# Optimization experiments

Hardware: AMD Instinct MI355X
Metric: run time of the kernel (lower is better)

The kernel has to match this reference:

```python
import jax, jax.numpy as jnp
import numpy as np

N_HEADS = 16
D_EMBED = 1024
N_CROSS = 768
D_HEAD = D_EMBED // N_HEADS


def setup_inputs() -> dict:
    key = jax.random.key(0)
    ks = jax.random.split(key, 10)
    B, S = 2, 2048
    x = jax.random.normal(ks[0], (B, S, D_EMBED), dtype=jnp.float32)
    context = jax.random.normal(ks[1], (B, S, N_CROSS), dtype=jnp.float32)
    sq = 1.0 / np.sqrt(D_EMBED)
    sc = 1.0 / np.sqrt(N_CROSS)
    Wq = jax.random.normal(ks[2], (D_EMBED, D_EMBED), dtype=jnp.float32) * sq
    bq = jnp.zeros((D_EMBED,), dtype=jnp.float32)
    Wk = jax.random.normal(ks[3], (N_CROSS, D_EMBED), dtype=jnp.float32) * sc
    bk = jnp.zeros((D_EMBED,), dtype=jnp.float32)
    Wv = jax.random.normal(ks[4], (N_CROSS, D_EMBED), dtype=jnp.float32) * sc
    bv = jnp.zeros((D_EMBED,), dtype=jnp.float32)
    Wo = jax.random.normal(ks[5], (D_EMBED, D_EMBED), dtype=jnp.float32) * sq
    bo = jnp.zeros((D_EMBED,), dtype=jnp.float32)
    return {"x": x, "context": context, "Wq": Wq, "bq": bq, "Wk": Wk, "bk": bk,
            "Wv": Wv, "bv": bv, "Wo": Wo, "bo": bo}


def reference(x, context, Wq, bq, Wk, bk, Wv, bv, Wo, bo):
    B, S, _ = x.shape

    def split_heads(t):  # [B,S,E] -> [B,H,S,Dh]
        return t.reshape(B, S, N_HEADS, D_HEAD).transpose(0, 2, 1, 3)

    q = split_heads(x @ Wq + bq)
    k = split_heads(context @ Wk + bk)
    v = split_heads(context @ Wv + bv)

    scale = 1.0 / np.sqrt(D_HEAD)
    scores = jnp.einsum('bhqd,bhkd->bhqk', q, k) * scale
    attn = jax.nn.softmax(scores, axis=-1)
    out = jnp.einsum('bhqk,bhkd->bhqd', attn, v)
    out = out.transpose(0, 2, 1, 3).reshape(B, S, D_EMBED)
    return out @ Wo + bo
```

## Files before the change

### kernel.cpp

```cpp
#include <hip/hip_runtime.h>
#include <math.h>


namespace {

typedef short bfr __attribute__((ext_vector_type(8)));
typedef short s4v __attribute__((ext_vector_type(4)));
typedef unsigned u4v __attribute__((ext_vector_type(4)));
typedef float accf __attribute__((ext_vector_type(16)));

#define MFMA32(a, b, c) __builtin_amdgcn_mfma_f32_32x32x16_bf16(a, b, c, 0, 0, 0)

__device__ inline short f2bf(float f) {
    unsigned u = __float_as_uint(f);
    u += 0x7fffu + ((u >> 16) & 1u);
    return (short)(u >> 16);
}
__device__ inline float bf2f(short s) {
    return __uint_as_float(((unsigned)(unsigned short)s) << 16);
}
__device__ inline float fexp2(float x) { return __builtin_amdgcn_exp2f(x); }
__device__ inline accf zero16() {
    accf z;
#pragma unroll
    for (int i = 0; i < 16; ++i) z[i] = 0.f;
    return z;
}
__device__ inline void dma16(const void* g, void* l) {
    __builtin_amdgcn_global_load_lds(
        (const __attribute__((address_space(1))) void*)g,
        (__attribute__((address_space(3))) void*)l, 16, 0, 0);
}

__global__ __launch_bounds__(256) void prep(
    const float* __restrict__ x, const float* __restrict__ ctx,
    short* __restrict__ xb, short* __restrict__ cb,
    const float* __restrict__ Wq, const float* __restrict__ Wk,
    const float* __restrict__ Wv, const float* __restrict__ Wo,
    short* __restrict__ Wqt, short* __restrict__ Wkt,
    short* __restrict__ Wvt, short* __restrict__ Wot) {
    __shared__ short t[64][68];
    const int bx = blockIdx.x;
    if (bx < 7168) {
        int i = bx * 256 + threadIdx.x;
        if (i < 1048576) {
            float4 v = ((const float4*)x)[i];
            s4v p = {f2bf(v.x), f2bf(v.y), f2bf(v.z), f2bf(v.w)};
            ((s4v*)xb)[i] = p;
        } else {
            int j = i - 1048576;
            float4 v = ((const float4*)ctx)[j];
            s4v p = {f2bf(v.x), f2bf(v.y), f2bf(v.z), f2bf(v.w)};
            ((s4v*)cb)[j] = p;
        }
        return;
    }
    const int idx = bx - 7168;
    const int z = idx >> 8, gy = (idx >> 4) & 15, gx = idx & 15;
    const float* W;
    short* Wt;
    int K;
    switch (z) {
        case 0: W = Wq; Wt = Wqt; K = 1024; break;
        case 1: W = Wk; Wt = Wkt; K = 768; break;
        case 2: W = Wv; Wt = Wvt; K = 768; break;
        default: W = Wo; Wt = Wot; K = 1024; break;
    }
    const int k0 = gy * 64;
    if (k0 >= K) return;
    const int tid = threadIdx.x;
    const int n0 = gx * 64;
    const int kr = tid >> 4, nc = (tid & 15) * 4;
#pragma unroll
    for (int rep = 0; rep < 4; ++rep) {
        int k = kr + rep * 16;
        float4 v = *(const float4*)&W[(size_t)(k0 + k) * 1024 + n0 + nc];
        t[nc + 0][k] = f2bf(v.x);
        t[nc + 1][k] = f2bf(v.y);
        t[nc + 2][k] = f2bf(v.z);
        t[nc + 3][k] = f2bf(v.w);
    }
    __syncthreads();
    const int nr = tid >> 4, kc = (tid & 15) * 4;
#pragma unroll
    for (int rep = 0; rep < 4; ++rep) {
        int n = nr + rep * 16;
        s4v p = {t[n][kc], t[n][kc + 1], t[n][kc + 2], t[n][kc + 3]};
        *(s4v*)&Wt[(size_t)(n0 + n) * K + k0 + kc] = p;
    }
}

__global__ __launch_bounds__(512, 6) void gemm_qkv(
    const short* __restrict__ xb, const short* __restrict__ cb,
    const short* __restrict__ Wqt, const short* __restrict__ Wkt,
    const short* __restrict__ Wvt, const float* __restrict__ bq,
    const float* __restrict__ bk, const float* __restrict__ bv,
    short* __restrict__ Qf, short* __restrict__ Kf, short* __restrict__ Vt,
    float qscale) {
    const int bid = blockIdx.x;
    const int z = bid >> 8;
    const int local = bid & 255;
    const short* A  = (z == 0) ? xb : cb;
    const short* Bt = (z == 0) ? Wqt : ((z == 1) ? Wkt : Wvt);
    const float* bias = (z == 0) ? bq : ((z == 1) ? bk : bv);
    const int K = (z == 0) ? 1024 : 768;
    const int NIT = K / 32;
    const float scale = (z == 0) ? qscale : 1.f;
    short* out = (z == 0) ? Qf : ((z == 1) ? Kf : Vt);

    __shared__ short As[12288];
    __shared__ short Bs[12288];
    const int t = threadIdx.x, lane = t & 63, w = t >> 6;
    const int lm = lane & 31, h2 = lane >> 5;
    const int wm = w & 1, wn = w >> 1;
    const int m0 = (local & 31) * 128, n0 = (local >> 5) * 128;

    const int st = t ^ ((t >> 3) & 7);
    const int srow = st >> 2, scol = (st & 3) * 8;
    const short* ga = A + (size_t)(m0 + srow) * K + scol;
    const short* gb = Bt + (size_t)(n0 + srow) * K + scol;

    const int xorv = (lm >> 1) & 7;
    const int rA0 = wm * 64 + lm, rB0 = wn * 32 + lm;

    accf acc[2] = {zero16(), zero16()};

    dma16(ga, &As[w * 512]);
    dma16(gb, &Bs[w * 512]);
    __builtin_amdgcn_sched_barrier(0);
    dma16(ga + 32, &As[4096 + w * 512]);
    dma16(gb + 32, &Bs[4096 + w * 512]);
    __builtin_amdgcn_sched_barrier(0);

    int buf = 0;
#pragma unroll 1
    for (int it = 0; it < NIT; ++it) {
        __builtin_amdgcn_sched_barrier(0);
        asm volatile("s_waitcnt vmcnt(2)" ::: "memory");
        __builtin_amdgcn_s_barrier();
        __builtin_amdgcn_sched_barrier(0);
        {
            const int nx = (it + 2 >= NIT) ? (it + 2 - NIT) : (it + 2);
            const int nb = (buf + 2 >= 3) ? (buf - 1) : (buf + 2);
            dma16(ga + nx * 32, &As[nb * 4096 + w * 512]);
            dma16(gb + nx * 32, &Bs[nb * 4096 + w * 512]);
        }
        const short* bA = &As[buf * 4096];
        const short* bB = &Bs[buf * 4096];
#pragma unroll
        for (int kk8 = 0; kk8 < 4; kk8 += 2) {
            bfr a0 = *(const bfr*)&bA[((rA0 * 4 + h2 + kk8) ^ xorv) * 8];
            bfr a1 = *(const bfr*)&bA[(((rA0 + 32) * 4 + h2 + kk8) ^ xorv) * 8];
            bfr b0 = *(const bfr*)&bB[((rB0 * 4 + h2 + kk8) ^ xorv) * 8];
            acc[0] = MFMA32(a0, b0, acc[0]);
            acc[1] = MFMA32(a1, b0, acc[1]);
        }
        buf = (buf + 1 == 3) ? 0 : buf + 1;
    }
    asm volatile("s_waitcnt vmcnt(0)" ::: "memory");
    __builtin_amdgcn_sched_barrier(0);

    const int n = n0 + wn * 32 + lm;
    const float bn = bias[n];
    const int hh = n >> 6, dd = n & 63;
#pragma unroll
    for (int mt = 0; mt < 2; ++mt) {
        const int mbase = m0 + wm * 64 + mt * 32 + 4 * h2;
        if (z != 2) {
            const int cb2 = (dd >> 4) * 512 + ((dd >> 3) & 1) * 256 + (dd & 7);
#pragma unroll
            for (int r = 0; r < 16; ++r) {
                const int m = mbase + (r & 3) + 8 * (r >> 2);
                const int bb = m >> 11, q = m & 2047;
                float v = (acc[mt][r] + bn) * scale;
                out[((size_t)((bb * 16 + hh) * 64 + (q >> 5))) * 2048 +
                    cb2 + (q & 31) * 8] = f2bf(v);
            }
        } else {
            const int dblk = dd >> 5, lmv = dd & 31;
#pragma unroll
            for (int g = 0; g < 4; ++g) {
                const int m = mbase + 8 * g;
                const int bb = m >> 11, s = m & 2047;
                const int kvt = s >> 6, kc = (s >> 4) & 3;
                const int h2v = (s >> 3) & 1, j0 = s & 7;
                s4v pq = {f2bf(acc[mt][4 * g + 0] + bn),
                          f2bf(acc[mt][4 * g + 1] + bn),
                          f2bf(acc[mt][4 * g + 2] + bn),
                          f2bf(acc[mt][4 * g + 3] + bn)};
                *(s4v*)(out +
                        ((size_t)(((bb * 16 + hh) * 32 + kvt) * 2 + dblk)) * 2048 +
                        kc * 512 + h2v * 256 + lmv * 8 + j0) = pq;
            }
        }
    }
}

__global__ __launch_bounds__(256) void combine(
    short* __restrict__ p0, const short* __restrict__ p1,
    const float* __restrict__ lsum) {
    const int i = blockIdx.x * 256 + threadIdx.x;
    const size_t gi = (size_t)i * 8;
    const int row = (int)(gi >> 10), col = (int)(gi & 1023);
    const int h = col >> 6;
    const int b = row >> 11, q = row & 2047;
    const float l0 = lsum[((size_t)b * 16 + h) * 2048 + q];
    const float l1 = lsum[((size_t)(2 + b) * 16 + h) * 2048 + q];
    const float iv = 1.f / (l0 + l1);
    bfr v0 = *(const bfr*)(p0 + gi);
    bfr v1 = *(const bfr*)(p1 + gi);
    bfr pk;
#pragma unroll
    for (int j = 0; j < 8; ++j)
        pk[j] = f2bf((bf2f(v0[j]) + bf2f(v1[j])) * iv);
    *(bfr*)(p0 + gi) = pk;
}

__global__ __launch_bounds__(512, 6) void gemm_o(
    const short* __restrict__ Af, const short* __restrict__ Bt,
    const float* __restrict__ bias, float* __restrict__ out) {
    constexpr int K = 1024, NIT = 32;
    __shared__ short As[12288];
    __shared__ short Bs[12288];
    const int t = threadIdx.x, lane = t & 63, w = t >> 6;
    const int lm = lane & 31, h2 = lane >> 5;
    const int wm = w & 1, wn = w >> 1;
    const int bid = blockIdx.x;
    const int m0 = (bid & 31) * 128, n0 = (bid >> 5) * 128;

    const int st = t ^ ((t >> 3) & 7);
    const int srow = st >> 2, scol = (st & 3) * 8;
    const short* ga = Af + (size_t)(m0 + srow) * K + scol;
    const short* gb = Bt + (size_t)(n0 + srow) * K + scol;

    const int xorv = (lm >> 1) & 7;
    const int rA0 = wm * 64 + lm, rB0 = wn * 32 + lm;

    accf acc[2] = {zero16(), zero16()};

    dma16(ga, &As[w * 512]);
    dma16(gb, &Bs[w * 512]);
    __builtin_amdgcn_sched_barrier(0);
    dma16(ga + 32, &As[4096 + w * 512]);
    dma16(gb + 32, &Bs[4096 + w * 512]);
    __builtin_amdgcn_sched_barrier(0);

    int buf = 0;
#pragma unroll 1
    for (int it = 0; it < NIT; ++it) {
        __builtin_amdgcn_sched_barrier(0);
        asm volatile("s_waitcnt vmcnt(2)" ::: "memory");
        __builtin_amdgcn_s_barrier();
        __builtin_amdgcn_sched_barrier(0);
        {
            const int nx = (it + 2 >= NIT) ? (it + 2 - NIT) : (it + 2);
            const int nb = (buf + 2 >= 3) ? (buf - 1) : (buf + 2);
            dma16(ga + nx * 32, &As[nb * 4096 + w * 512]);
            dma16(gb + nx * 32, &Bs[nb * 4096 + w * 512]);
        }
        const short* bA = &As[buf * 4096];
        const short* bB = &Bs[buf * 4096];
#pragma unroll
        for (int kk8 = 0; kk8 < 4; kk8 += 2) {
            bfr a0 = *(const bfr*)&bA[((rA0 * 4 + h2 + kk8) ^ xorv) * 8];
            bfr a1 = *(const bfr*)&bA[(((rA0 + 32) * 4 + h2 + kk8) ^ xorv) * 8];
            bfr b0 = *(const bfr*)&bB[((rB0 * 4 + h2 + kk8) ^ xorv) * 8];
            acc[0] = MFMA32(a0, b0, acc[0]);
            acc[1] = MFMA32(a1, b0, acc[1]);
        }
        buf = (buf + 1 == 3) ? 0 : buf + 1;
    }
    asm volatile("s_waitcnt vmcnt(0)" ::: "memory");
    __builtin_amdgcn_sched_barrier(0);

    const int n = n0 + wn * 32 + lm;
    const float bn = bias[n];
#pragma unroll
    for (int mt = 0; mt < 2; ++mt) {
        const int mbase = m0 + wm * 64 + mt * 32 + 4 * h2;
#pragma unroll
        for (int r = 0; r < 16; ++r) {
            const int m = mbase + (r & 3) + 8 * (r >> 2);
            out[(size_t)m * 1024 + n] = acc[mt][r] + bn;
        }
    }
}

__global__ __launch_bounds__(256, 3) void attn(
    const short* __restrict__ Qf, const short* __restrict__ Kf,
    const short* __restrict__ Vt, short* __restrict__ part,
    float* __restrict__ lsum) {
    __shared__ short smem[16384];
    const int bid = blockIdx.x;
    const int hidx = bid & 31, qs = bid >> 5;
    const int split = qs & 1, qb = qs >> 1;
    const int b = hidx >> 4, h = hidx & 15;
    const int lane = threadIdx.x & 63, wv = threadIdx.x >> 6;
    const int lm = lane & 31, h2 = lane >> 5;
    const bool hb = h2 != 0;
    const int q0 = qb * 128 + wv * 32;

    const short* qbase =
        Qf + ((size_t)(hidx * 64 + (q0 >> 5))) * 2048 + lane * 8;
    bfr qf[4];
#pragma unroll
    for (int kc = 0; kc < 4; ++kc) qf[kc] = *(const bfr*)(qbase + kc * 512);

    const short* khead = Kf + (size_t)hidx * 131072 + split * 65536;
    const short* vhead = Vt + (size_t)hidx * 131072 + split * 65536;
    const short* gsrc =
        ((wv < 2) ? (khead + wv * 2048) : (vhead + (wv - 2) * 2048)) + lane * 8;

#pragma unroll
    for (int i = 0; i < 4; ++i)
        dma16(gsrc + i * 512, &smem[wv * 2048 + i * 512]);

    accf oa0 = zero16(), oa1 = zero16();
    float la0 = 0.f, la1 = 0.f;

#pragma unroll 1
    for (int it = 0; it < 16; ++it) {
        const int p = it & 1;
        __syncthreads();
        if (it + 1 < 16) {
            const short* gn = gsrc + (size_t)(it + 1) * 4096;
            short* ln = &smem[(1 - p) * 8192 + wv * 2048];
#pragma unroll
            for (int i = 0; i < 4; ++i) dma16(gn + i * 512, ln + i * 512);
        }
        const short* kb = &smem[p * 8192];
        bfr kf0[4], kf1[4], vf0[4], vf1[4];
#pragma unroll
        for (int kc = 0; kc < 4; ++kc) {
            kf0[kc] = *(const bfr*)&kb[kc * 512 + lane * 8];
            kf1[kc] = *(const bfr*)&kb[2048 + kc * 512 + lane * 8];
            vf0[kc] = *(const bfr*)&kb[4096 + kc * 512 + lane * 8];
            vf1[kc] = *(const bfr*)&kb[6144 + kc * 512 + lane * 8];
        }
        accf s0 = zero16(), s1 = zero16();
#pragma unroll
        for (int kc = 0; kc < 4; ++kc) {
            s0 = MFMA32(kf0[kc], qf[kc], s0);
            s1 = MFMA32(kf1[kc], qf[kc], s1);
        }

#pragma unroll
        for (int i = 0; i < 16; ++i) s0[i] = fexp2(s0[i]);
#pragma unroll
        for (int i = 0; i < 16; ++i) s1[i] = fexp2(s1[i]);
#pragma unroll
        for (int i = 0; i < 16; ++i) {
            if (i & 1) la1 += s0[i] + s1[i];
            else       la0 += s0[i] + s1[i];
        }

        bfr pb[4];
#pragma unroll
        for (int kc = 0; kc < 4; ++kc) {
            const accf& s = (kc < 2) ? s0 : s1;
            const int base = 8 * (kc & 1);
            unsigned Lw0 = __builtin_amdgcn_perm(__float_as_uint(s[base + 1]),
                                                 __float_as_uint(s[base + 0]),
                                                 0x07060302u);
            unsigned Lw1 = __builtin_amdgcn_perm(__float_as_uint(s[base + 3]),
                                                 __float_as_uint(s[base + 2]),
                                                 0x07060302u);
            unsigned Hw0 = __builtin_amdgcn_perm(__float_as_uint(s[base + 5]),
                                                 __float_as_uint(s[base + 4]),
                                                 0x07060302u);
            unsigned Hw1 = __builtin_amdgcn_perm(__float_as_uint(s[base + 7]),
                                                 __float_as_uint(s[base + 6]),
                                                 0x07060302u);
            unsigned c0 = hb ? Lw0 : Hw0;
            unsigned c1 = hb ? Lw1 : Hw1;
            unsigned r0 = (unsigned)__shfl_xor((int)c0, 32);
            unsigned r1 = (unsigned)__shfl_xor((int)c1, 32);
            u4v pw = {hb ? r0 : Lw0, hb ? r1 : Lw1,
                      hb ? Hw0 : r0, hb ? Hw1 : r1};
            pb[kc] = __builtin_bit_cast(bfr, pw);
        }

#pragma unroll
        for (int kc = 0; kc < 4; ++kc) {
            oa0 = MFMA32(vf0[kc], pb[kc], oa0);
            oa1 = MFMA32(vf1[kc], pb[kc], oa1);
        }
    }

    float ls = la0 + la1;
    ls += __shfl_xor(ls, 32);
    if (!hb) lsum[((size_t)(split * 2 + b) * 16 + h) * 2048 + q0 + lm] = ls;

    short* orow = part + (size_t)split * 4194304 +
                  (size_t)(b * 2048 + q0 + lm) * 1024 + h * 64;
#pragma unroll
    for (int dt = 0; dt < 2; ++dt) {
        const accf& oa = dt ? oa1 : oa0;
#pragma unroll
        for (int g = 0; g < 4; ++g) {
            const int d0 = dt * 32 + 4 * h2 + 8 * g;
            s4v p = {f2bf(oa[4 * g + 0]), f2bf(oa[4 * g + 1]),
                     f2bf(oa[4 * g + 2]), f2bf(oa[4 * g + 3])};
            *(s4v*)(orow + d0) = p;
        }
    }
}

}

extern "C" void kernel_launch(void* const* d_in, const int* in_sizes, int n_in,
                              void* d_out, int out_size, void* d_ws,
                              size_t ws_size, hipStream_t stream) {
    const float* x   = (const float*)d_in[0];
    const float* ctx = (const float*)d_in[1];
    const float* Wq  = (const float*)d_in[2];
    const float* bq  = (const float*)d_in[3];
    const float* Wk  = (const float*)d_in[4];
    const float* bk  = (const float*)d_in[5];
    const float* Wv  = (const float*)d_in[6];
    const float* bv  = (const float*)d_in[7];
    const float* Wo  = (const float*)d_in[8];
    const float* bo  = (const float*)d_in[9];

    short* xb  = (short*)d_ws;
    short* cb  = xb + (size_t)4096 * 1024;
    short* Wqt = cb + (size_t)4096 * 768;
    short* Wkt = Wqt + (size_t)1024 * 1024;
    short* Wvt = Wkt + (size_t)1024 * 768;
    short* Wot = Wvt + (size_t)1024 * 768;
    short* Qf  = Wot + (size_t)1024 * 1024;
    short* Kf  = Qf + (size_t)4096 * 1024;
    short* Vt  = Kf + (size_t)4096 * 1024;
    short* p0  = Vt + (size_t)4096 * 1024;
    short* p1  = p0 + (size_t)4096 * 1024;
    float* lsum = (float*)(p1 + (size_t)4096 * 1024);

    prep<<<8192, 256, 0, stream>>>(x, ctx, xb, cb, Wq, Wk, Wv, Wo,
                                   Wqt, Wkt, Wvt, Wot);

    const float qscale = 0.125f * 1.44269504088896f;
    gemm_qkv<<<768, 512, 0, stream>>>(xb, cb, Wqt, Wkt, Wvt,
                                      bq, bk, bv, Qf, Kf, Vt, qscale);

    attn<<<1024, 256, 0, stream>>>(Qf, Kf, Vt, p0, lsum);

    combine<<<2048, 256, 0, stream>>>(p0, p1, lsum);

    gemm_o<<<256, 512, 0, stream>>>(p0, Wot, bo, (float*)d_out);
}
```

Baseline: 203.5 us.

## Drop KV-split attention and combine kernel; halve gemm_o N tile

The attention kernel no longer splits the key/value sequence in two. Each block now walks the full 2048 keys and normalizes by its own softmax sum, so the separate combine kernel and its partial-buffer traffic are gone. The grid shrinks to 512 blocks with longer serial loops, which may hurt occupancy and latency hiding. gemm_o switches to 128x64 tiles with one MFMA accumulator per wave and 512 blocks, giving more parallelism but less reuse per load.

```diff
diff --git a/kernel.cpp b/kernel.cpp
--- a/kernel.cpp
+++ b/kernel.cpp
@@ -196,77 +196,60 @@
     }
 }
 
-__global__ __launch_bounds__(256) void combine(
-    short* __restrict__ p0, const short* __restrict__ p1,
-    const float* __restrict__ lsum) {
-    const int i = blockIdx.x * 256 + threadIdx.x;
-    const size_t gi = (size_t)i * 8;
-    const int row = (int)(gi >> 10), col = (int)(gi & 1023);
-    const int h = col >> 6;
-    const int b = row >> 11, q = row & 2047;
-    const float l0 = lsum[((size_t)b * 16 + h) * 2048 + q];
-    const float l1 = lsum[((size_t)(2 + b) * 16 + h) * 2048 + q];
-    const float iv = 1.f / (l0 + l1);
-    bfr v0 = *(const bfr*)(p0 + gi);
-    bfr v1 = *(const bfr*)(p1 + gi);
-    bfr pk;
-#pragma unroll
-    for (int j = 0; j < 8; ++j)
-        pk[j] = f2bf((bf2f(v0[j]) + bf2f(v1[j])) * iv);
-    *(bfr*)(p0 + gi) = pk;
-}
-
 __global__ __launch_bounds__(512, 6) void gemm_o(
     const short* __restrict__ Af, const short* __restrict__ Bt,
     const float* __restrict__ bias, float* __restrict__ out) {
     constexpr int K = 1024, NIT = 32;
     __shared__ short As[12288];
-    __shared__ short Bs[12288];
+    __shared__ short Bs[6144];
     const int t = threadIdx.x, lane = t & 63, w = t >> 6;
     const int lm = lane & 31, h2 = lane >> 5;
-    const int wm = w & 1, wn = w >> 1;
+    const int wm = w & 3, wn = w >> 2;
     const int bid = blockIdx.x;
-    const int m0 = (bid & 31) * 128, n0 = (bid >> 5) * 128;
+    const int m0 = (bid & 31) * 128, n0 = (bid >> 5) * 64;
 
     const int st = t ^ ((t >> 3) & 7);
     const int srow = st >> 2, scol = (st & 3) * 8;
     const short* ga = Af + (size_t)(m0 + srow) * K + scol;
     const short* gb = Bt + (size_t)(n0 + srow) * K + scol;
+    const bool bw = (w < 4);
 
     const int xorv = (lm >> 1) & 7;
-    const int rA0 = wm * 64 + lm, rB0 = wn * 32 + lm;
-
-    accf acc[2] = {zero16(), zero16()};
+    const int rA0 = wm * 32 + lm, rB0 = wn * 32 + lm;
+
+    accf acc = zero16();
 
     dma16(ga, &As[w * 512]);
-    dma16(gb, &Bs[w * 512]);
+    if (bw) dma16(gb, &Bs[w * 512]);
     __builtin_amdgcn_sched_barrier(0);
     dma16(ga + 32, &As[4096 + w * 512]);
-    dma16(gb + 32, &Bs[4096 + w * 512]);
+    if (bw) dma16(gb + 32, &Bs[2048 + w * 512]);
     __builtin_amdgcn_sched_barrier(0);
 
     int buf = 0;
 #pragma unroll 1
     for (int it = 0; it < NIT; ++it) {
         __builtin_amdgcn_sched_barrier(0);
-        asm volatile("s_waitcnt vmcnt(2)" ::: "memory");
+        if (bw) {
+            asm volatile("s_waitcnt vmcnt(2)" ::: "memory");
+        } else {
+            asm volatile("s_waitcnt vmcnt(1)" ::: "memory");
+        }
         __builtin_amdgcn_s_barrier();
         __builtin_amdgcn_sched_barrier(0);
         {
             const int nx = (it + 2 >= NIT) ? (it + 2 - NIT) : (it + 2);
             const int nb = (buf + 2 >= 3) ? (buf - 1) : (buf + 2);
             dma16(ga + nx * 32, &As[nb * 4096 + w * 512]);
-            dma16(gb + nx * 32, &Bs[nb * 4096 + w * 512]);
+            if (bw) dma16(gb + nx * 32, &Bs[nb * 2048 + w * 512]);
         }
         const short* bA = &As[buf * 4096];
-        const short* bB = &Bs[buf * 4096];
+        const short* bB = &Bs[buf * 2048];
 #pragma unroll
         for (int kk8 = 0; kk8 < 4; kk8 += 2) {
             bfr a0 = *(const bfr*)&bA[((rA0 * 4 + h2 + kk8) ^ xorv) * 8];
-            bfr a1 = *(const bfr*)&bA[(((rA0 + 32) * 4 + h2 + kk8) ^ xorv) * 8];
             bfr b0 = *(const bfr*)&bB[((rB0 * 4 + h2 + kk8) ^ xorv) * 8];
-            acc[0] = MFMA32(a0, b0, acc[0]);
-            acc[1] = MFMA32(a1, b0, acc[1]);
+            acc = MFMA32(a0, b0, acc);
         }
         buf = (buf + 1 == 3) ? 0 : buf + 1;
     }
@@ -275,25 +258,20 @@
 
     const int n = n0 + wn * 32 + lm;
     const float bn = bias[n];
-#pragma unroll
-    for (int mt = 0; mt < 2; ++mt) {
-        const int mbase = m0 + wm * 64 + mt * 32 + 4 * h2;
-#pragma unroll
-        for (int r = 0; r < 16; ++r) {
-            const int m = mbase + (r & 3) + 8 * (r >> 2);
-            out[(size_t)m * 1024 + n] = acc[mt][r] + bn;
-        }
+    const int mbase = m0 + wm * 32 + 4 * h2;
+#pragma unroll
+    for (int r = 0; r < 16; ++r) {
+        const int m = mbase + (r & 3) + 8 * (r >> 2);
+        out[(size_t)m * 1024 + n] = acc[r] + bn;
     }
 }
 
 __global__ __launch_bounds__(256, 3) void attn(
     const short* __restrict__ Qf, const short* __restrict__ Kf,
-    const short* __restrict__ Vt, short* __restrict__ part,
-    float* __restrict__ lsum) {
+    const short* __restrict__ Vt, short* __restrict__ part) {
     __shared__ short smem[16384];
     const int bid = blockIdx.x;
-    const int hidx = bid & 31, qs = bid >> 5;
-    const int split = qs & 1, qb = qs >> 1;
+    const int hidx = bid & 31, qb = bid >> 5;
     const int b = hidx >> 4, h = hidx & 15;
     const int lane = threadIdx.x & 63, wv = threadIdx.x >> 6;
     const int lm = lane & 31, h2 = lane >> 5;
@@ -306,8 +284,8 @@
 #pragma unroll
     for (int kc = 0; kc < 4; ++kc) qf[kc] = *(const bfr*)(qbase + kc * 512);
 
-    const short* khead = Kf + (size_t)hidx * 131072 + split * 65536;
-    const short* vhead = Vt + (size_t)hidx * 131072 + split * 65536;
+    const short* khead = Kf + (size_t)hidx * 131072;
+    const short* vhead = Vt + (size_t)hidx * 131072;
     const short* gsrc =
         ((wv < 2) ? (khead + wv * 2048) : (vhead + (wv - 2) * 2048)) + lane * 8;
 
@@ -319,10 +297,10 @@
     float la0 = 0.f, la1 = 0.f;
 
 #pragma unroll 1
-    for (int it = 0; it < 16; ++it) {
+    for (int it = 0; it < 32; ++it) {
         const int p = it & 1;
         __syncthreads();
-        if (it + 1 < 16) {
+        if (it + 1 < 32) {
             const short* gn = gsrc + (size_t)(it + 1) * 4096;
             short* ln = &smem[(1 - p) * 8192 + wv * 2048];
 #pragma unroll
@@ -389,18 +367,17 @@
 
     float ls = la0 + la1;
     ls += __shfl_xor(ls, 32);
-    if (!hb) lsum[((size_t)(split * 2 + b) * 16 + h) * 2048 + q0 + lm] = ls;
-
-    short* orow = part + (size_t)split * 4194304 +
-                  (size_t)(b * 2048 + q0 + lm) * 1024 + h * 64;
+    const float iv = 1.f / ls;
+
+    short* orow = part + (size_t)(b * 2048 + q0 + lm) * 1024 + h * 64;
 #pragma unroll
     for (int dt = 0; dt < 2; ++dt) {
         const accf& oa = dt ? oa1 : oa0;
 #pragma unroll
         for (int g = 0; g < 4; ++g) {
             const int d0 = dt * 32 + 4 * h2 + 8 * g;
-            s4v p = {f2bf(oa[4 * g + 0]), f2bf(oa[4 * g + 1]),
-                     f2bf(oa[4 * g + 2]), f2bf(oa[4 * g + 3])};
+            s4v p = {f2bf(oa[4 * g + 0] * iv), f2bf(oa[4 * g + 1] * iv),
+                     f2bf(oa[4 * g + 2] * iv), f2bf(oa[4 * g + 3] * iv)};
             *(s4v*)(orow + d0) = p;
         }
     }
@@ -432,8 +409,6 @@
     short* Kf  = Qf + (size_t)4096 * 1024;
     short* Vt  = Kf + (size_t)4096 * 1024;
     short* p0  = Vt + (size_t)4096 * 1024;
-    short* p1  = p0 + (size_t)4096 * 1024;
-    float* lsum = (float*)(p1 + (size_t)4096 * 1024);
 
     prep<<<8192, 256, 0, stream>>>(x, ctx, xb, cb, Wq, Wk, Wv, Wo,
                                    Wqt, Wkt, Wvt, Wot);
@@ -442,9 +417,7 @@
     gemm_qkv<<<768, 512, 0, stream>>>(xb, cb, Wqt, Wkt, Wvt,
                                       bq, bk, bv, Qf, Kf, Vt, qscale);
 
-    attn<<<1024, 256, 0, stream>>>(Qf, Kf, Vt, p0, lsum);
-
-    combine<<<2048, 256, 0, stream>>>(p0, p1, lsum);
-
-    gemm_o<<<256, 512, 0, stream>>>(p0, Wot, bo, (float*)d_out);
-}
+    attn<<<512, 256, 0, stream>>>(Qf, Kf, Vt, p0);
+
+    gemm_o<<<512, 512, 0, stream>>>(p0, Wot, bo, (float*)d_out);
+}
```

Measured after the change: 199.3 us, median of 4. 2.1% less time.
